# Performance work log

Hardware: AMD Instinct MI355X
Metric: run time of the kernel (lower is better)

The kernel has to match this reference:

```python
import jax, jax.numpy as jnp
import numpy as np

# ---- static config (mirrors init_kwargs) ----
BATCH = 16384
N_SCALARS = 64
N_KERNELS = 32
L2_INDICES = tuple(range(15))
N_L2 = len(L2_INDICES) + 1          # selected kernels + sum-over-kernels
HIDDEN_MIX = 256
HIDDEN_CORR = 128
SILU_NORM = 1.6790                   # e3nn normalize2mom constant for silu

# ---- real-basis Wigner 3j tensors (unit Frobenius norm, as in e3nn) ----
def _su2_gen(l):
    m = np.arange(-l, l + 1)
    d = 2 * l + 1
    Jz = np.diag(m).astype(complex)
    jp = np.sqrt(l * (l + 1) - m[:-1] * (m[:-1] + 1))
    Jp = np.zeros((d, d), complex)
    Jp[np.arange(1, d), np.arange(0, d - 1)] = jp
    Jm = Jp.conj().T
    return (Jp + Jm) / 2, (Jp - Jm) / 2j, Jz

def _real_basis(l):
    d = 2 * l + 1
    U = np.zeros((d, d), complex)
    U[l, l] = 1.0
    for m in range(1, l + 1):
        U[l + m, l + m] = (-1) ** m / np.sqrt(2)
        U[l + m, l - m] = 1 / np.sqrt(2)
        U[l - m, l - m] = 1j / np.sqrt(2)
        U[l - m, l + m] = -1j * (-1) ** m / np.sqrt(2)
    return U

def _real_gens(l):
    if l == 0:
        return [np.zeros((1, 1))] * 3
    U = _real_basis(l)
    return [np.real(U @ (-1j * J) @ U.conj().T) for J in _su2_gen(l)]

def _w3j(l1, l2, l3):
    G1, G2, G3 = _real_gens(l1), _real_gens(l2), _real_gens(l3)
    d1, d2, d3 = 2 * l1 + 1, 2 * l2 + 1, 2 * l3 + 1
    I1, I2, I3 = np.eye(d1), np.eye(d2), np.eye(d3)
    rows = []
    for a in range(3):  # invariance under all 3 so(3) generators
        rows.append(np.kron(np.kron(G1[a], I2), I3)
                    + np.kron(np.kron(I1, G2[a]), I3)
                    + np.kron(np.kron(I1, I2), G3[a]))
    M = np.concatenate(rows, 0)
    _, _, Vh = np.linalg.svd(M)
    c = Vh[-1].reshape(d1, d2, d3)
    c = c / np.linalg.norm(c)
    idx = np.unravel_index(np.argmax(np.abs(c)), c.shape)
    return (c * np.sign(c[idx])).astype(np.float32)

C000 = jnp.asarray(_w3j(0, 0, 0))
C022 = jnp.asarray(_w3j(0, 2, 2))
C202 = jnp.asarray(_w3j(2, 0, 2))
C220 = jnp.asarray(_w3j(2, 2, 0))
C222 = jnp.asarray(_w3j(2, 2, 2))

def _tp_path(w, c, x1, x2):
    # w: [u,v,w], c (wigner 3j): [i,j,k], x1: [b,u,i], x2: [b,v,j] -> [b,w,k]
    return jnp.einsum('uvw,ijk,bui,bvj->bwk', w, c, x1, x2, optimize='optimal')

def _forward(scalars, kernel_t2s, mlp_w1, mlp_w2, mlp_w3, gate_threshold,
             tp1_w000, tp1_w220, tp1_w022, tp1_w202, tp1_w222,
             tp2_w022, tp2_w202, tp2_w222, correction_scale):
    # ---- KernelMixingHead ----
    h = SILU_NORM * jax.nn.silu(scalars @ mlp_w1 / mlp_w1.shape[0] ** 0.5)
    h = SILU_NORM * jax.nn.silu(h @ mlp_w2 / mlp_w2.shape[0] ** 0.5)
    relative = h @ mlp_w3 / mlp_w3.shape[0] ** 0.5          # [B, K]
    magnitude = jnp.linalg.norm(kernel_t2s, axis=-1)         # [B, K]
    gate = magnitude / (magnitude + gate_threshold)
    weights = relative * gate / N_KERNELS ** 0.5
    mixed = jnp.einsum('bk,bkm->bm', weights, kernel_t2s)    # [B, 5]

    # ---- EquivariantCorrectionHead ----
    sel = kernel_t2s[:, jnp.asarray(L2_INDICES), :]          # [B, n_l2-1, 5]
    t = jnp.concatenate([sel, kernel_t2s.sum(axis=1, keepdims=True)], axis=1)  # [B, N_L2, 5]
    xs = scalars[:, :, None]                                 # [B, ns, 1] (0e channels)
    ns, nl, hc = N_SCALARS, N_L2, HIDDEN_CORR
    # e3nn FullyConnectedTensorProduct path norms ('component'/'element')
    a0 = (1.0 / (ns * ns + nl * nl)) ** 0.5
    a2 = (5.0 / (2 * ns * nl + nl * nl)) ** 0.5
    y0 = a0 * (_tp_path(tp1_w000, C000, xs, xs) + _tp_path(tp1_w220, C220, t, t))   # [B,hc,1]
    y2 = a2 * (_tp_path(tp1_w022, C022, xs, t) + _tp_path(tp1_w202, C202, t, xs)
               + _tp_path(tp1_w222, C222, t, t))                                     # [B,hc,5]
    b2 = (5.0 / (3 * hc * hc)) ** 0.5
    corr = b2 * (_tp_path(tp2_w022, C022, y0, y2) + _tp_path(tp2_w202, C202, y2, y0)
                 + _tp_path(tp2_w222, C222, y2, y2))                                 # [B,1,5]
    return mixed + correction_scale * corr[:, 0, :]

def setup_inputs() -> dict:
    key = jax.random.key(0)
    ks = jax.random.split(key, 13)
    f32 = jnp.float32
    return {
        'scalars': jax.random.normal(ks[0], (BATCH, N_SCALARS), f32),
        'kernel_t2s': jax.random.normal(ks[1], (BATCH, N_KERNELS, 5), f32),
        'mlp_w1': jax.random.normal(ks[2], (N_SCALARS, HIDDEN_MIX), f32),
        'mlp_w2': jax.random.normal(ks[3], (HIDDEN_MIX, HIDDEN_MIX), f32),
        'mlp_w3': jax.random.normal(ks[4], (HIDDEN_MIX, N_KERNELS), f32),
        'gate_threshold': jnp.ones((N_KERNELS,), f32),
        'tp1_w000': jax.random.normal(ks[5], (N_SCALARS, N_SCALARS, HIDDEN_CORR), f32),
        'tp1_w220': jax.random.normal(ks[6], (N_L2, N_L2, HIDDEN_CORR), f32),
        'tp1_w022': jax.random.normal(ks[7], (N_SCALARS, N_L2, HIDDEN_CORR), f32),
        'tp1_w202': jax.random.normal(ks[8], (N_L2, N_SCALARS, HIDDEN_CORR), f32),
        'tp1_w222': jax.random.normal(ks[9], (N_L2, N_L2, HIDDEN_CORR), f32),
        'tp2_w022': jax.random.normal(ks[10], (HIDDEN_CORR, HIDDEN_CORR, 1), f32),
        'tp2_w202': jax.random.normal(ks[11], (HIDDEN_CORR, HIDDEN_CORR, 1), f32),
        'tp2_w222': jax.random.normal(ks[12], (HIDDEN_CORR, HIDDEN_CORR, 1), f32),
        'correction_scale': jnp.asarray(0.1, f32),
    }

def reference(scalars, kernel_t2s, mlp_w1, mlp_w2, mlp_w3, gate_threshold,
              tp1_w000, tp1_w220, tp1_w022, tp1_w202, tp1_w222,
              tp2_w022, tp2_w202, tp2_w222, correction_scale):
    return _forward(scalars, kernel_t2s, mlp_w1, mlp_w2, mlp_w3, gate_threshold,
                    tp1_w000, tp1_w220, tp1_w022, tp1_w202, tp1_w222,
                    tp2_w022, tp2_w202, tp2_w222, correction_scale)
```

## Files before the change

kernel.cpp:

```cpp
#include <hip/hip_runtime.h>
#include <hip/hip_bf16.h>
#include <cmath>
#include <complex>
#include <vector>
#include <cstring>
#include <cstdint>


#define C222_FLIP -1.0f

#define MIX_WS_OFF   0
#define W202T_OFF    327680
#define B2H_OFF      393216
#define B2L_OFF      1294336
#define Y0_WS_OFF    2195456
#define Y2P_OFF      10584064

#define NCHUNK2      110

typedef __attribute__((ext_vector_type(8))) short short8;
typedef __attribute__((ext_vector_type(4))) float f32x4;

struct Coefs {
  float c222[125];
  float d022[5];
  float d202[5];
  float d220[5];
  float a0, a2, b2;
};

#define FMA8(acc, wa, wb, sv) do { \
  acc[0] = fmaf((wa).x, (sv), acc[0]); \
  acc[1] = fmaf((wa).y, (sv), acc[1]); \
  acc[2] = fmaf((wa).z, (sv), acc[2]); \
  acc[3] = fmaf((wa).w, (sv), acc[3]); \
  acc[4] = fmaf((wb).x, (sv), acc[4]); \
  acc[5] = fmaf((wb).y, (sv), acc[5]); \
  acc[6] = fmaf((wb).z, (sv), acc[6]); \
  acc[7] = fmaf((wb).w, (sv), acc[7]); \
} while (0)

#define FMA4(acc, wa, sv) do { \
  acc[0] = fmaf((wa).x, (sv), acc[0]); \
  acc[1] = fmaf((wa).y, (sv), acc[1]); \
  acc[2] = fmaf((wa).z, (sv), acc[2]); \
  acc[3] = fmaf((wa).w, (sv), acc[3]); \
} while (0)

__device__ __forceinline__ float act_silu(float x) {
  return 1.679f * x / (1.0f + expf(-x));
}

__device__ __forceinline__ short f2bf(float x) {
  __hip_bfloat16 h = __float2bfloat16(x);
  return *reinterpret_cast<short*>(&h);
}
__device__ __forceinline__ float bf2f(short s) {
  __hip_bfloat16 h = *reinterpret_cast<__hip_bfloat16*>(&s);
  return __bfloat162float(h);
}

__device__ __forceinline__ int bperm(int n, int k) {
  return ((n >> 4) << 9) | (((((k >> 3) << 4) | (n & 15))) << 3) | (k & 7);
}

__global__ __launch_bounds__(256) void k_prep(
    const float* __restrict__ s, const float* __restrict__ t2s,
    const float* __restrict__ w1, const float* __restrict__ w2,
    const float* __restrict__ w3, const float* __restrict__ gthr,
    float* __restrict__ mixed_ws)
{
  __shared__ float sT[64][36];
  __shared__ float hT[256][36];

  const int tid = threadIdx.x;
  const int b0  = blockIdx.x * 32;

  #pragma unroll
  for (int i = 0; i < 8; i++) {
    int flat = tid + i * 256;
    int bl = flat >> 6, k = flat & 63;
    sT[k][bl] = s[(size_t)(b0 + bl) * 64 + k];
  }
  __syncthreads();

  const int cg = tid & 31, bg = tid >> 5;
  const int c0 = cg * 8, bb0 = bg * 4;

  float acc[4][8];
  #pragma unroll
  for (int j = 0; j < 4; j++)
    #pragma unroll
    for (int i = 0; i < 8; i++) acc[j][i] = 0.f;

  for (int k = 0; k < 64; k++) {
    float4 bv = *(const float4*)&sT[k][bb0];
    float4 wa = *(const float4*)&w1[k * 256 + c0];
    float4 wb = *(const float4*)&w1[k * 256 + c0 + 4];
    const float bvv[4] = {bv.x, bv.y, bv.z, bv.w};
    #pragma unroll
    for (int j = 0; j < 4; j++) { FMA8(acc[j], wa, wb, bvv[j]); }
  }
  #pragma unroll
  for (int j = 0; j < 4; j++)
    #pragma unroll
    for (int i = 0; i < 8; i++)
      hT[c0 + i][bb0 + j] = act_silu(acc[j][i] * 0.125f);
  __syncthreads();

  float acc2[4][8];
  #pragma unroll
  for (int j = 0; j < 4; j++)
    #pragma unroll
    for (int i = 0; i < 8; i++) acc2[j][i] = 0.f;

  for (int k = 0; k < 256; k++) {
    float4 bv = *(const float4*)&hT[k][bb0];
    float4 wa = *(const float4*)&w2[k * 256 + c0];
    float4 wb = *(const float4*)&w2[k * 256 + c0 + 4];
    const float bvv[4] = {bv.x, bv.y, bv.z, bv.w};
    #pragma unroll
    for (int j = 0; j < 4; j++) { FMA8(acc2[j], wa, wb, bvv[j]); }
  }
  __syncthreads();
  #pragma unroll
  for (int j = 0; j < 4; j++)
    #pragma unroll
    for (int i = 0; i < 8; i++)
      hT[c0 + i][bb0 + j] = act_silu(acc2[j][i] * 0.0625f);
  __syncthreads();

  const int jj  = tid & 31;
  const int blg = tid >> 5;
  float acc3[4] = {0.f, 0.f, 0.f, 0.f};
  for (int k = 0; k < 256; k++) {
    float wv  = w3[k * 32 + jj];
    float4 hv = *(const float4*)&hT[k][blg * 4];
    acc3[0] = fmaf(hv.x, wv, acc3[0]);
    acc3[1] = fmaf(hv.y, wv, acc3[1]);
    acc3[2] = fmaf(hv.z, wv, acc3[2]);
    acc3[3] = fmaf(hv.w, wv, acc3[3]);
  }
  const float thrv = gthr[jj];
  #pragma unroll
  for (int r = 0; r < 4; r++) {
    int bl = blg * 4 + r;
    int b  = b0 + bl;
    float rel = acc3[r] * 0.0625f;
    const float* tp = t2s + (size_t)(b * 32 + jj) * 5;
    float tv0 = tp[0], tv1 = tp[1], tv2 = tp[2], tv3 = tp[3], tv4 = tp[4];
    float mag  = sqrtf(tv0*tv0 + tv1*tv1 + tv2*tv2 + tv3*tv3 + tv4*tv4);
    float gate = mag / (mag + thrv);
    float w = rel * gate * 0.17677669529663687f;
    float pm0 = w*tv0, pm1 = w*tv1, pm2 = w*tv2, pm3 = w*tv3, pm4 = w*tv4;
    #pragma unroll
    for (int off = 16; off >= 1; off >>= 1) {
      pm0 += __shfl_xor(pm0, off);
      pm1 += __shfl_xor(pm1, off);
      pm2 += __shfl_xor(pm2, off);
      pm3 += __shfl_xor(pm3, off);
      pm4 += __shfl_xor(pm4, off);
    }
    if (jj == 0) {
      float* mp = mixed_ws + (size_t)b * 5;
      mp[0] = pm0; mp[1] = pm1; mp[2] = pm2; mp[3] = pm3; mp[4] = pm4;
    }
  }
}

__global__ __launch_bounds__(256) void k_wprep(
    const float* __restrict__ w000,
    const float* __restrict__ w2202, float* __restrict__ w202T,
    const float* __restrict__ w022, const float* __restrict__ w202,
    const float* __restrict__ w222, const float* __restrict__ w220,
    short* __restrict__ B2h, short* __restrict__ B2l)
{
  const int tid = threadIdx.x;
  const int blk = blockIdx.x;
  if (blk < 64) {
    int u = blk;
    int base = u * 64 - (u * (u - 1)) / 2;
    int n = (64 - u) * 128;
    for (int idx = tid; idx < n; idx += 256) {
      int t = idx >> 7, wc = idx & 127;
      int v = u + t;
      int p = base + t;
      float val = w000[(size_t)(u * 64 + v) * 128 + wc];
      if (v > u) val += w000[(size_t)(v * 64 + u) * 128 + wc];
      size_t off = (size_t)(45 + (p >> 5)) * 4096 + bperm(wc, p & 31);
      short hs = f2bf(val);
      B2h[off] = hs;
      B2l[off] = f2bf(val - bf2f(hs));
    }
  } else if (blk < 128) {
    int idx = (blk - 64) * 256 + tid;
    int u = idx >> 7, v = idx & 127;
    w202T[v * 128 + u] = w2202[u * 128 + v];
  } else {
    int c = blk - 128;
    #pragma unroll
    for (int i = 0; i < 16; i++) {
      int e = i * 256 + tid;
      int nb = e >> 9;
      int ln = (e >> 3) & 63;
      int j  = e & 7;
      int w  = nb * 16 + (ln & 15);
      int kk = ((ln >> 4) << 3) | j;
      float V = 0.f;
      if (c < 32) {
        int v = c >> 1, u = (c & 1) * 32 + kk;
        V = w022[(size_t)(u * 16 + v) * 128 + w]
          + w202[(size_t)(v * 64 + u) * 128 + w];
      } else if (c < 40) {
        int K = (c - 32) * 32 + kk;
        int u = K >> 4, v = K & 15;
        V = w222[(size_t)(u * 16 + v) * 128 + w];
      } else {
        int q = (c - 40) * 32 + kk;
        if (q < 136) {
          int u = 0;
          while ((u + 1) * 16 - ((u + 1) * u) / 2 <= q) u++;
          int base = u * 16 - (u * (u - 1)) / 2;
          int v = u + (q - base);
          V = w220[(size_t)(u * 16 + v) * 128 + w];
          if (v > u) V += w220[(size_t)(v * 16 + u) * 128 + w];
        }
      }
      short hs = f2bf(V);
      B2h[(size_t)c * 4096 + e] = hs;
      B2l[(size_t)c * 4096 + e] = f2bf(V - bf2f(hs));
    }
  }
}

__global__ __launch_bounds__(512) void k_y2a(
    const float* __restrict__ s, const float* __restrict__ t2s,
    const short* __restrict__ B2h, const short* __restrict__ B2l,
    unsigned short* __restrict__ y2p, Coefs cf)
{
  __shared__ float sL[64][68];
  __shared__ float tL[64][81];
  __shared__ __align__(16) short BhL[2][4096];
  __shared__ __align__(16) short BlL[2][4096];
  __shared__ float cL222[125];

  const int tid  = threadIdx.x;
  const int b0   = blockIdx.x * 64;
  const int wave = tid >> 6;
  const int lane = tid & 63;
  const int m16  = lane & 15;
  const int quad = lane >> 4;
  const int bg   = wave & 3;
  const int nh   = wave >> 2;
  const int bloc = bg * 16 + m16;
  const int wbase = nh * 64;

  float dk022[5];
  #pragma unroll
  for (int k = 0; k < 5; k++) dk022[k] = cf.d022[k];

  if (tid == 0) {
    #pragma unroll
    for (int i = 0; i < 125; i++) cL222[i] = cf.c222[i];
  }
  for (int idx = tid; idx < 4096; idx += 512) {
    int bl = idx >> 6, k = idx & 63;
    sL[bl][k] = s[(size_t)(b0 + bl) * 64 + k];
  }
  for (int idx = tid; idx < 5120; idx += 512) {
    int bl = idx / 80, rem = idx - bl * 80;
    int u = rem / 5, m = rem - u * 5;
    int b = b0 + bl;
    float v;
    if (u < 15) v = t2s[(size_t)(b * 32 + u) * 5 + m];
    else {
      v = 0.f;
      for (int kk = 0; kk < 32; kk++) v += t2s[(size_t)(b * 32 + kk) * 5 + m];
    }
    tL[bl][rem] = v;
  }
  __syncthreads();

  ((short8*)BhL[0])[tid] = ((const short8*)B2h)[tid];
  ((short8*)BlL[0])[tid] = ((const short8*)B2l)[tid];
  __syncthreads();

  f32x4 acc[5][4];
  #pragma unroll
  for (int k = 0; k < 5; k++)
    #pragma unroll
    for (int nf = 0; nf < 4; nf++) acc[k][nf] = 0.f;
  f32x4 p[4];
  #pragma unroll
  for (int nf = 0; nf < 4; nf++) p[nf] = 0.f;

  for (int c = 0; c < 40; c++) {
    const int cur = c & 1;
    if (c + 1 < 40) {
      ((short8*)BhL[cur ^ 1])[tid] = ((const short8*)(B2h + (size_t)(c + 1) * 4096))[tid];
      ((short8*)BlL[cur ^ 1])[tid] = ((const short8*)(B2l + (size_t)(c + 1) * 4096))[tid];
    }
    short8 bhv[4], blv[4];
    #pragma unroll
    for (int nf = 0; nf < 4; nf++) {
      const int nb = nh * 4 + nf;
      bhv[nf] = *(const short8*)&BhL[cur][nb * 512 + lane * 8];
      blv[nf] = *(const short8*)&BlL[cur][nb * 512 + lane * 8];
    }

    if (c < 32) {
      const int ks = c & 1;
      float sv[8];
      {
        float4 a = *(const float4*)&sL[bloc][ks * 32 + quad * 8];
        float4 b = *(const float4*)&sL[bloc][ks * 32 + quad * 8 + 4];
        sv[0]=a.x; sv[1]=a.y; sv[2]=a.z; sv[3]=a.w;
        sv[4]=b.x; sv[5]=b.y; sv[6]=b.z; sv[7]=b.w;
      }
      short8 ah, al;
      #pragma unroll
      for (int j = 0; j < 8; j++) {
        float x = sv[j];
        short hs = f2bf(x);
        ah[j] = hs;
        al[j] = f2bf(x - bf2f(hs));
      }
      #pragma unroll
      for (int nf = 0; nf < 4; nf++) {
        p[nf] = __builtin_amdgcn_mfma_f32_16x16x32_bf16(ah, bhv[nf], p[nf], 0, 0, 0);
        p[nf] = __builtin_amdgcn_mfma_f32_16x16x32_bf16(ah, blv[nf], p[nf], 0, 0, 0);
        p[nf] = __builtin_amdgcn_mfma_f32_16x16x32_bf16(al, bhv[nf], p[nf], 0, 0, 0);
      }
      if (ks == 1) {
        const int v = c >> 1;
        #pragma unroll
        for (int r = 0; r < 4; r++) {
          const int bl = bg * 16 + quad * 4 + r;
          const float* tr = &tL[bl][v * 5];
          #pragma unroll
          for (int k = 0; k < 5; k++) {
            float f = dk022[k] * tr[k];
            #pragma unroll
            for (int nf = 0; nf < 4; nf++)
              acc[k][nf][r] += f * p[nf][r];
          }
        }
        #pragma unroll
        for (int nf = 0; nf < 4; nf++) p[nf] = 0.f;
      }
    } else {
      int cc = c - 32;
      int u  = cc * 2 + (quad >> 1);
      int vb = (quad & 1) * 8;
      float tu[5];
      #pragma unroll
      for (int i = 0; i < 5; i++) tu[i] = tL[bloc][u * 5 + i];
      float G[25];
      #pragma unroll
      for (int jk = 0; jk < 25; jk++) {
        float g = 0.f;
        #pragma unroll
        for (int i = 0; i < 5; i++)
          g = fmaf(cL222[i * 25 + jk], tu[i], g);
        G[jk] = g;
      }
      float av[5][8];
      #pragma unroll
      for (int j = 0; j < 8; j++) {
        float t5[5];
        #pragma unroll
        for (int j5 = 0; j5 < 5; j5++) t5[j5] = tL[bloc][(vb + j) * 5 + j5];
        #pragma unroll
        for (int k = 0; k < 5; k++) {
          float q = 0.f;
          #pragma unroll
          for (int j5 = 0; j5 < 5; j5++)
            q = fmaf(G[j5 * 5 + k], t5[j5], q);
          av[k][j] = q;
        }
      }
      #pragma unroll
      for (int k = 0; k < 5; k++) {
        short8 ah, al;
        #pragma unroll
        for (int j = 0; j < 8; j++) {
          float x = av[k][j];
          short hs = f2bf(x);
          ah[j] = hs;
          al[j] = f2bf(x - bf2f(hs));
        }
        #pragma unroll
        for (int nf = 0; nf < 4; nf++) {
          acc[k][nf] = __builtin_amdgcn_mfma_f32_16x16x32_bf16(ah, bhv[nf], acc[k][nf], 0, 0, 0);
          acc[k][nf] = __builtin_amdgcn_mfma_f32_16x16x32_bf16(ah, blv[nf], acc[k][nf], 0, 0, 0);
          acc[k][nf] = __builtin_amdgcn_mfma_f32_16x16x32_bf16(al, bhv[nf], acc[k][nf], 0, 0, 0);
        }
      }
    }
    __syncthreads();
  }

  #pragma unroll
  for (int nf = 0; nf < 4; nf++) {
    int ch = wbase + nf * 16 + m16;
    #pragma unroll
    for (int r = 0; r < 4; r++) {
      int b = b0 + bg * 16 + quad * 4 + r;
      #pragma unroll
      for (int k = 0; k < 5; k++)
        y2p[((size_t)b * 5 + k) * 128 + ch] = (unsigned short)f2bf(acc[k][nf][r]);
    }
  }
}

__global__ __launch_bounds__(512) void k_y0b(
    const float* __restrict__ s, const float* __restrict__ t2s,
    const short* __restrict__ B2h, const short* __restrict__ B2l,
    float* __restrict__ y0w, Coefs cf)
{
  __shared__ float sL[64][68];
  __shared__ float tL[64][81];
  __shared__ __align__(16) short BhL[2][4096];
  __shared__ __align__(16) short BlL[2][4096];
  __shared__ unsigned char p136s[136];
  __shared__ unsigned short p16[2080];

  const int tid  = threadIdx.x;
  const int b0   = blockIdx.x * 64;
  const int wave = tid >> 6;
  const int lane = tid & 63;
  const int m16  = lane & 15;
  const int quad = lane >> 4;
  const int bg   = wave & 3;
  const int nh   = wave >> 2;
  const int bloc = bg * 16 + m16;
  const int wbase = nh * 64;

  float dk220[5];
  #pragma unroll
  for (int k = 0; k < 5; k++) dk220[k] = cf.d220[k];

  for (int idx = tid; idx < 4096; idx += 512) {
    int bl = idx >> 6, k = idx & 63;
    sL[bl][k] = s[(size_t)(b0 + bl) * 64 + k];
  }
  for (int idx = tid; idx < 5120; idx += 512) {
    int bl = idx / 80, rem = idx - bl * 80;
    int u = rem / 5, m = rem - u * 5;
    int b = b0 + bl;
    float v;
    if (u < 15) v = t2s[(size_t)(b * 32 + u) * 5 + m];
    else {
      v = 0.f;
      for (int kk = 0; kk < 32; kk++) v += t2s[(size_t)(b * 32 + kk) * 5 + m];
    }
    tL[bl][rem] = v;
  }
  if (tid < 16) {
    int u = tid;
    int base = u * 16 - (u * (u - 1)) / 2;
    for (int t = 0; t < 16 - u; t++)
      p136s[base + t] = (unsigned char)((u << 4) | (u + t));
  }
  if (tid < 64) {
    int u = tid;
    int base = u * 64 - (u * (u - 1)) / 2;
    for (int t = 0; t < 64 - u; t++)
      p16[base + t] = (unsigned short)((u << 8) | (u + t));
  }
  __syncthreads();

  ((short8*)BhL[0])[tid] = ((const short8*)(B2h + (size_t)40 * 4096))[tid];
  ((short8*)BlL[0])[tid] = ((const short8*)(B2l + (size_t)40 * 4096))[tid];
  __syncthreads();

  f32x4 accY0[4];
  #pragma unroll
  for (int nf = 0; nf < 4; nf++) accY0[nf] = 0.f;

  for (int c = 40; c < NCHUNK2; c++) {
    const int cur = c & 1;
    if (c + 1 < NCHUNK2) {
      ((short8*)BhL[cur ^ 1])[tid] = ((const short8*)(B2h + (size_t)(c + 1) * 4096))[tid];
      ((short8*)BlL[cur ^ 1])[tid] = ((const short8*)(B2l + (size_t)(c + 1) * 4096))[tid];
    }
    short8 bhv[4], blv[4];
    #pragma unroll
    for (int nf = 0; nf < 4; nf++) {
      const int nb = nh * 4 + nf;
      bhv[nf] = *(const short8*)&BhL[cur][nb * 512 + lane * 8];
      blv[nf] = *(const short8*)&BlL[cur][nb * 512 + lane * 8];
    }

    short8 ah, al;
    if (c < 45) {
      int cc = c - 40;
      int qbase = cc * 32 + quad * 8;
      #pragma unroll
      for (int j = 0; j < 8; j++) {
        int q = qbase + j;
        float g = 0.f;
        if (q < 136) {
          int uv = p136s[q];
          int u = uv >> 4, v = uv & 15;
          #pragma unroll
          for (int m = 0; m < 5; m++)
            g = fmaf(dk220[m] * tL[bloc][u * 5 + m], tL[bloc][v * 5 + m], g);
        }
        short hs = f2bf(g);
        ah[j] = hs;
        al[j] = f2bf(g - bf2f(hs));
      }
    } else {
      int pbase = (c - 45) * 32 + quad * 8;
      #pragma unroll
      for (int j = 0; j < 8; j++) {
        int uv = p16[pbase + j];
        float x = sL[bloc][uv >> 8] * sL[bloc][uv & 255];
        short hs = f2bf(x);
        ah[j] = hs;
        al[j] = f2bf(x - bf2f(hs));
      }
    }
    #pragma unroll
    for (int nf = 0; nf < 4; nf++) {
      accY0[nf] = __builtin_amdgcn_mfma_f32_16x16x32_bf16(ah, bhv[nf], accY0[nf], 0, 0, 0);
      accY0[nf] = __builtin_amdgcn_mfma_f32_16x16x32_bf16(ah, blv[nf], accY0[nf], 0, 0, 0);
      accY0[nf] = __builtin_amdgcn_mfma_f32_16x16x32_bf16(al, bhv[nf], accY0[nf], 0, 0, 0);
    }
    __syncthreads();
  }

  #pragma unroll
  for (int nf = 0; nf < 4; nf++) {
    int ch = wbase + nf * 16 + m16;
    #pragma unroll
    for (int r = 0; r < 4; r++) {
      int b = b0 + bg * 16 + quad * 4 + r;
      y0w[(size_t)b * 128 + ch] = accY0[nf][r];
    }
  }
}

__global__ __launch_bounds__(512) void k_fused(
    const float* __restrict__ mixed_ws,
    const float* __restrict__ y0w, const unsigned short* __restrict__ y2p,
    const float* __restrict__ w2022, const float* __restrict__ w202T,
    const float* __restrict__ w2222,
    const float* __restrict__ csc, float* __restrict__ out, Coefs cf)
{
  __shared__ __align__(16) float y0I[16][128][2];
  __shared__ __align__(16) float wLd[32][128];
  __shared__ float y2S[5][16][32][2];
  __shared__ float cL222[125];
  __shared__ float corrAcc[32][5];
  __shared__ float pPL[32][25];

  const int tid = threadIdx.x;
  const int b0  = blockIdx.x * 32;

  float dk022[5], dk202[5];
  #pragma unroll
  for (int k = 0; k < 5; k++) { dk022[k] = cf.d022[k]; dk202[k] = cf.d202[k]; }

  if (tid == 0) {
    #pragma unroll
    for (int i = 0; i < 125; i++) cL222[i] = cf.c222[i];
  }
  for (int idx = tid; idx < 4096; idx += 512) {
    int bl = idx >> 7, ch = idx & 127;
    y0I[bl >> 1][ch][bl & 1] = cf.a0 * y0w[(size_t)(b0 + bl) * 128 + ch];
  }

  const int xw = tid & 31;
  const int g  = tid >> 5;
  const int w0 = xw * 4;
  const int bA = 2 * g, bB = 2 * g + 1;
  const int srow = tid >> 4;
  const int scol = (tid & 15) * 8;

  float y2acc[5][2][4];
  #pragma unroll
  for (int k = 0; k < 5; k++) {
    #pragma unroll
    for (int h = 0; h < 2; h++) {
      int b = b0 + 2 * g + h;
      const unsigned short* yp = y2p + ((size_t)b * 5 + k) * 128 + w0;
      ushort4 u4 = *(const ushort4*)yp;
      y2acc[k][h][0] = cf.a2 * bf2f((short)u4.x);
      y2acc[k][h][1] = cf.a2 * bf2f((short)u4.y);
      y2acc[k][h][2] = cf.a2 * bf2f((short)u4.z);
      y2acc[k][h][3] = cf.a2 * bf2f((short)u4.w);
    }
  }
  __syncthreads();

  {
    float gvr[2][4] = {{0.f,0.f,0.f,0.f},{0.f,0.f,0.f,0.f}};
    for (int t = 0; t < 4; t++) {
      const int u0 = t * 32;
      *(float4*)&wLd[srow][scol]     = *(const float4*)(w2022 + (size_t)(u0 + srow) * 128 + scol);
      *(float4*)&wLd[srow][scol + 4] = *(const float4*)(w2022 + (size_t)(u0 + srow) * 128 + scol + 4);
      __syncthreads();
      #pragma unroll 8
      for (int uu = 0; uu < 32; uu++) {
        float2 y0p = *(const float2*)&y0I[g][u0 + uu][0];
        float4 w4 = *(const float4*)&wLd[uu][w0];
        FMA4(gvr[0], w4, y0p.x);
        FMA4(gvr[1], w4, y0p.y);
      }
      __syncthreads();
    }
    #pragma unroll
    for (int k = 0; k < 5; k++) {
      float pA = gvr[0][0]*y2acc[k][0][0] + gvr[0][1]*y2acc[k][0][1]
               + gvr[0][2]*y2acc[k][0][2] + gvr[0][3]*y2acc[k][0][3];
      float pB = gvr[1][0]*y2acc[k][1][0] + gvr[1][1]*y2acc[k][1][1]
               + gvr[1][2]*y2acc[k][1][2] + gvr[1][3]*y2acc[k][1][3];
      pA += __shfl_xor(pA, 16); pA += __shfl_xor(pA, 8); pA += __shfl_xor(pA, 4);
      pA += __shfl_xor(pA, 2);  pA += __shfl_xor(pA, 1);
      pB += __shfl_xor(pB, 16); pB += __shfl_xor(pB, 8); pB += __shfl_xor(pB, 4);
      pB += __shfl_xor(pB, 2);  pB += __shfl_xor(pB, 1);
      if (xw == 0) {
        corrAcc[bA][k] = dk022[k] * pA;
        corrAcc[bB][k] = dk022[k] * pB;
      }
    }
  }
  {
    float hvr[2][4] = {{0.f,0.f,0.f,0.f},{0.f,0.f,0.f,0.f}};
    for (int t = 0; t < 4; t++) {
      const int u0 = t * 32;
      *(float4*)&wLd[srow][scol]     = *(const float4*)(w202T + (size_t)(u0 + srow) * 128 + scol);
      *(float4*)&wLd[srow][scol + 4] = *(const float4*)(w202T + (size_t)(u0 + srow) * 128 + scol + 4);
      __syncthreads();
      #pragma unroll 8
      for (int uu = 0; uu < 32; uu++) {
        float2 y0p = *(const float2*)&y0I[g][u0 + uu][0];
        float4 w4 = *(const float4*)&wLd[uu][w0];
        FMA4(hvr[0], w4, y0p.x);
        FMA4(hvr[1], w4, y0p.y);
      }
      __syncthreads();
    }
    #pragma unroll
    for (int k = 0; k < 5; k++) {
      float pA = hvr[0][0]*y2acc[k][0][0] + hvr[0][1]*y2acc[k][0][1]
               + hvr[0][2]*y2acc[k][0][2] + hvr[0][3]*y2acc[k][0][3];
      float pB = hvr[1][0]*y2acc[k][1][0] + hvr[1][1]*y2acc[k][1][1]
               + hvr[1][2]*y2acc[k][1][2] + hvr[1][3]*y2acc[k][1][3];
      pA += __shfl_xor(pA, 16); pA += __shfl_xor(pA, 8); pA += __shfl_xor(pA, 4);
      pA += __shfl_xor(pA, 2);  pA += __shfl_xor(pA, 1);
      pB += __shfl_xor(pB, 16); pB += __shfl_xor(pB, 8); pB += __shfl_xor(pB, 4);
      pB += __shfl_xor(pB, 2);  pB += __shfl_xor(pB, 1);
      if (xw == 0) {
        corrAcc[bA][k] += dk202[k] * pA;
        corrAcc[bB][k] += dk202[k] * pB;
      }
    }
  }
  {
    float zr[5][2][4];
    #pragma unroll
    for (int i = 0; i < 5; i++)
      #pragma unroll
      for (int h = 0; h < 2; h++)
        #pragma unroll
        for (int w = 0; w < 4; w++) zr[i][h][w] = 0.f;

    for (int t = 0; t < 4; t++) {
      const int u0 = t * 32;
      *(float4*)&wLd[srow][scol]     = *(const float4*)(w2222 + (size_t)(u0 + srow) * 128 + scol);
      *(float4*)&wLd[srow][scol + 4] = *(const float4*)(w2222 + (size_t)(u0 + srow) * 128 + scol + 4);
      if (w0 >= u0 && w0 < u0 + 32) {
        const int uu0 = w0 - u0;
        #pragma unroll
        for (int i = 0; i < 5; i++)
          #pragma unroll
          for (int h = 0; h < 2; h++)
            #pragma unroll
            for (int c = 0; c < 4; c++)
              y2S[i][g][uu0 + c][h] = y2acc[i][h][c];
      }
      __syncthreads();
      #pragma unroll 4
      for (int uu = 0; uu < 32; uu++) {
        float4 w4 = *(const float4*)&wLd[uu][w0];
        #pragma unroll
        for (int i = 0; i < 5; i++) {
          float ya = y2S[i][g][uu][0];
          float yb = y2S[i][g][uu][1];
          FMA4(zr[i][0], w4, ya);
          FMA4(zr[i][1], w4, yb);
        }
      }
      __syncthreads();
    }
    #pragma unroll
    for (int i = 0; i < 5; i++) {
      #pragma unroll
      for (int j = 0; j < 5; j++) {
        float pA = zr[i][0][0]*y2acc[j][0][0] + zr[i][0][1]*y2acc[j][0][1]
                 + zr[i][0][2]*y2acc[j][0][2] + zr[i][0][3]*y2acc[j][0][3];
        float pB = zr[i][1][0]*y2acc[j][1][0] + zr[i][1][1]*y2acc[j][1][1]
                 + zr[i][1][2]*y2acc[j][1][2] + zr[i][1][3]*y2acc[j][1][3];
        pA += __shfl_xor(pA, 16); pA += __shfl_xor(pA, 8); pA += __shfl_xor(pA, 4);
        pA += __shfl_xor(pA, 2);  pA += __shfl_xor(pA, 1);
        pB += __shfl_xor(pB, 16); pB += __shfl_xor(pB, 8); pB += __shfl_xor(pB, 4);
        pB += __shfl_xor(pB, 2);  pB += __shfl_xor(pB, 1);
        if (xw == 0) {
          pPL[bA][i * 5 + j] = pA;
          pPL[bB][i * 5 + j] = pB;
        }
      }
    }
  }
  __syncthreads();

  if (tid < 160) {
    int bb = tid / 5, k = tid - bb * 5;
    float c2 = 0.f;
    #pragma unroll
    for (int ii = 0; ii < 5; ii++)
      #pragma unroll
      for (int jj = 0; jj < 5; jj++)
        c2 = fmaf(cL222[ii * 25 + jj * 5 + k], pPL[bb][ii * 5 + jj], c2);
    float tot = corrAcc[bb][k] + c2;
    int b = b0 + bb;
    out[(size_t)b * 5 + k] = mixed_ws[(size_t)b * 5 + k] + csc[0] * cf.b2 * tot;
  }
}

namespace {

using cplx = std::complex<double>;

static void su2_gen(int l, std::vector<cplx>& Jx, std::vector<cplx>& Jy,
                    std::vector<cplx>& Jz) {
  int d = 2 * l + 1;
  Jx.assign((size_t)d * d, cplx(0, 0));
  Jy.assign((size_t)d * d, cplx(0, 0));
  Jz.assign((size_t)d * d, cplx(0, 0));
  for (int a = 0; a < d; a++) Jz[(size_t)a * d + a] = cplx(a - l, 0);
  for (int r = 1; r < d; r++) {
    double m = (r - 1) - l;
    double v = std::sqrt(l * (l + 1.0) - m * (m + 1.0));
    Jx[(size_t)r * d + (r - 1)] += cplx(v / 2, 0);
    Jx[(size_t)(r - 1) * d + r] += cplx(v / 2, 0);
    Jy[(size_t)r * d + (r - 1)] += cplx(0, -v / 2);
    Jy[(size_t)(r - 1) * d + r] += cplx(0, v / 2);
  }
}

static void real_basis(int l, std::vector<cplx>& U) {
  int d = 2 * l + 1;
  U.assign((size_t)d * d, cplx(0, 0));
  U[(size_t)l * d + l] = cplx(1, 0);
  double is2 = 1.0 / std::sqrt(2.0);
  for (int m = 1; m <= l; m++) {
    double sgn = (m % 2 == 0) ? 1.0 : -1.0;
    U[(size_t)(l + m) * d + (l + m)] = cplx(sgn * is2, 0);
    U[(size_t)(l + m) * d + (l - m)] = cplx(is2, 0);
    U[(size_t)(l - m) * d + (l - m)] = cplx(0, is2);
    U[(size_t)(l - m) * d + (l + m)] = cplx(0, -sgn * is2);
  }
}

static void real_gens(int l, std::vector<double> G[3]) {
  int d = 2 * l + 1;
  if (l == 0) { for (int a = 0; a < 3; a++) G[a].assign(1, 0.0); return; }
  std::vector<cplx> J[3];
  su2_gen(l, J[0], J[1], J[2]);
  std::vector<cplx> U;
  real_basis(l, U);
  for (int a = 0; a < 3; a++) {
    std::vector<cplx> T((size_t)d * d, cplx(0, 0));
    for (int i = 0; i < d; i++)
      for (int k = 0; k < d; k++) {
        cplx s(0, 0);
        for (int j = 0; j < d; j++)
          s += U[(size_t)i * d + j] * (cplx(0, -1) * J[a][(size_t)j * d + k]);
        T[(size_t)i * d + k] = s;
      }
    G[a].assign((size_t)d * d, 0.0);
    for (int i = 0; i < d; i++)
      for (int k = 0; k < d; k++) {
        cplx s(0, 0);
        for (int j = 0; j < d; j++)
          s += T[(size_t)i * d + j] * std::conj(U[(size_t)k * d + j]);
        G[a][(size_t)i * d + k] = s.real();
      }
  }
}

static void w3j_host(int l1, int l2, int l3, float* out) {
  int d1 = 2 * l1 + 1, d2 = 2 * l2 + 1, d3 = 2 * l3 + 1;
  int D = d1 * d2 * d3;
  std::vector<double> G1[3], G2[3], G3[3];
  real_gens(l1, G1); real_gens(l2, G2); real_gens(l3, G3);
  int R = 3 * D;
  std::vector<double> M((size_t)R * D, 0.0);
  for (int a = 0; a < 3; a++) {
    double* Ma = &M[(size_t)a * D * D];
    for (int i1 = 0; i1 < d1; i1++)
      for (int j1 = 0; j1 < d1; j1++) {
        double g = G1[a][(size_t)i1 * d1 + j1];
        if (g == 0.0) continue;
        for (int i2 = 0; i2 < d2; i2++)
          for (int i3 = 0; i3 < d3; i3++)
            Ma[(size_t)((i1 * d2 + i2) * d3 + i3) * D + ((j1 * d2 + i2) * d3 + i3)] += g;
      }
    for (int i2 = 0; i2 < d2; i2++)
      for (int j2 = 0; j2 < d2; j2++) {
        double g = G2[a][(size_t)i2 * d2 + j2];
        if (g == 0.0) continue;
        for (int i1 = 0; i1 < d1; i1++)
          for (int i3 = 0; i3 < d3; i3++)
            Ma[(size_t)((i1 * d2 + i2) * d3 + i3) * D + ((i1 * d2 + j2) * d3 + i3)] += g;
      }
    for (int i3 = 0; i3 < d3; i3++)
      for (int j3 = 0; j3 < d3; j3++) {
        double g = G3[a][(size_t)i3 * d3 + j3];
        if (g == 0.0) continue;
        for (int i1 = 0; i1 < d1; i1++)
          for (int i2 = 0; i2 < d2; i2++)
            Ma[(size_t)((i1 * d2 + i2) * d3 + i3) * D + ((i1 * d2 + i2) * d3 + j3)] += g;
      }
  }
  std::vector<int> pivcol;
  int rank = 0;
  for (int col = 0; col < D && rank < R; col++) {
    int pr = -1; double pv = 1e-9;
    for (int r = rank; r < R; r++) {
      double av = std::fabs(M[(size_t)r * D + col]);
      if (av > pv) { pv = av; pr = r; }
    }
    if (pr < 0) continue;
    if (pr != rank)
      for (int c = 0; c < D; c++) std::swap(M[(size_t)pr * D + c], M[(size_t)rank * D + c]);
    double inv = 1.0 / M[(size_t)rank * D + col];
    for (int c = 0; c < D; c++) M[(size_t)rank * D + c] *= inv;
    for (int r = 0; r < R; r++) {
      if (r == rank) continue;
      double f = M[(size_t)r * D + col];
      if (f != 0.0)
        for (int c = 0; c < D; c++) M[(size_t)r * D + c] -= f * M[(size_t)rank * D + c];
    }
    pivcol.push_back(col);
    rank++;
  }
  std::vector<char> isp(D, 0);
  for (int c : pivcol) isp[c] = 1;
  int fc = 0;
  for (int c = 0; c < D; c++) if (!isp[c]) { fc = c; break; }
  std::vector<double> x(D, 0.0);
  x[fc] = 1.0;
  for (int r = 0; r < rank; r++) x[pivcol[r]] = -M[(size_t)r * D + fc];
  double n = 0;
  for (double v : x) n += v * v;
  n = std::sqrt(n);
  for (int c = 0; c < D; c++) x[c] /= n;
  double best = 0;
  for (int c = 0; c < D; c++) { double av = std::fabs(x[c]); if (av > best) best = av; }
  double ssum = 0;
  for (int c = 0; c < D; c++) {
    double av = std::fabs(x[c]);
    if (av >= best * 0.999) ssum += (x[c] >= 0 ? 1.0 : -1.0);
  }
  double sgn = (ssum >= 0) ? 1.0 : -1.0;
  for (int c = 0; c < D; c++) out[c] = (float)(x[c] * sgn);
}

}

extern "C" void kernel_launch(void* const* d_in, const int* in_sizes, int n_in,
                              void* d_out, int out_size, void* d_ws, size_t ws_size,
                              hipStream_t stream)
{
  (void)in_sizes; (void)n_in; (void)out_size; (void)ws_size;

  const float* s     = (const float*)d_in[0];
  const float* t2s   = (const float*)d_in[1];
  const float* w1    = (const float*)d_in[2];
  const float* w2    = (const float*)d_in[3];
  const float* w3    = (const float*)d_in[4];
  const float* gthr  = (const float*)d_in[5];
  const float* w000  = (const float*)d_in[6];
  const float* w220  = (const float*)d_in[7];
  const float* w022  = (const float*)d_in[8];
  const float* w202  = (const float*)d_in[9];
  const float* w222  = (const float*)d_in[10];
  const float* w2022 = (const float*)d_in[11];
  const float* w2202 = (const float*)d_in[12];
  const float* w2222 = (const float*)d_in[13];
  const float* csc   = (const float*)d_in[14];
  float* out = (float*)d_out;

  char* ws = (char*)d_ws;
  float* mixed_ws = (float*)(ws + MIX_WS_OFF);
  float* w202T    = (float*)(ws + W202T_OFF);
  short* B2h      = (short*)(ws + B2H_OFF);
  short* B2l      = (short*)(ws + B2L_OFF);
  float* y0_ws    = (float*)(ws + Y0_WS_OFF);
  unsigned short* y2p = (unsigned short*)(ws + Y2P_OFF);

  Coefs cf;
  {
    float c000v[1], c022v[25], c202v[25], c220v[25];
    w3j_host(0, 0, 0, c000v);
    w3j_host(0, 2, 2, c022v);
    w3j_host(2, 0, 2, c202v);
    w3j_host(2, 2, 0, c220v);
    w3j_host(2, 2, 2, cf.c222);
    for (int i = 0; i < 125; i++) cf.c222[i] *= C222_FLIP;
    for (int k = 0; k < 5; k++) {
      cf.d022[k] = c022v[k * 5 + k];
      cf.d202[k] = c202v[k * 5 + k];
      cf.d220[k] = c220v[k * 5 + k];
    }
    (void)c000v;
    cf.a0 = (float)std::sqrt(1.0 / (64.0 * 64.0 + 16.0 * 16.0));
    cf.a2 = (float)std::sqrt(5.0 / (2.0 * 64.0 * 16.0 + 16.0 * 16.0));
    cf.b2 = (float)std::sqrt(5.0 / (3.0 * 128.0 * 128.0));
  }

  hipLaunchKernelGGL(k_prep, dim3(512), dim3(256), 0, stream,
                     s, t2s, w1, w2, w3, gthr, mixed_ws);
  hipLaunchKernelGGL(k_wprep, dim3(173), dim3(256), 0, stream,
                     w000, w2202, w202T,
                     w022, w202, w222, w220, B2h, B2l);
  hipLaunchKernelGGL(k_y0b, dim3(256), dim3(512), 0, stream,
                     s, t2s, B2h, B2l, y0_ws, cf);
  hipLaunchKernelGGL(k_y2a, dim3(256), dim3(512), 0, stream,
                     s, t2s, B2h, B2l, y2p, cf);
  hipLaunchKernelGGL(k_fused, dim3(512), dim3(512), 0, stream,
                     mixed_ws, y0_ws, y2p, w2022, w202T, w2222, csc, out, cf);
}
```

Baseline: 403.4 us.

## Halve k_y0b batch tile, double grid, load B fragments directly from global

The y0 GEMM kernel now handles 32 batch rows per block instead of 64, so the grid doubles to 512 blocks. Each wave covers 32 output channels with two accumulators instead of four. The double-buffered LDS staging of B2h/B2l and the per-chunk __syncthreads are removed, and each wave reads its B fragments straight from global memory (L2-resident). The aim is more parallelism across CUs and no block-wide barriers, at the cost of more redundant global B reads and A-fragment recomputation per output.

```diff
diff --git a/kernel.cpp b/kernel.cpp
--- a/kernel.cpp
+++ b/kernel.cpp
@@ -418,33 +418,31 @@
     const short* __restrict__ B2h, const short* __restrict__ B2l,
     float* __restrict__ y0w, Coefs cf)
 {
-  __shared__ float sL[64][68];
-  __shared__ float tL[64][81];
-  __shared__ __align__(16) short BhL[2][4096];
-  __shared__ __align__(16) short BlL[2][4096];
+  __shared__ float sL[32][65];
+  __shared__ float tL[32][81];
   __shared__ unsigned char p136s[136];
   __shared__ unsigned short p16[2080];
 
   const int tid  = threadIdx.x;
-  const int b0   = blockIdx.x * 64;
+  const int b0   = blockIdx.x * 32;
   const int wave = tid >> 6;
   const int lane = tid & 63;
   const int m16  = lane & 15;
   const int quad = lane >> 4;
-  const int bg   = wave & 3;
-  const int nh   = wave >> 2;
+  const int bg   = wave & 1;
+  const int nh   = wave >> 1;
   const int bloc = bg * 16 + m16;
-  const int wbase = nh * 64;
+  const int wbase = nh * 32;
 
   float dk220[5];
   #pragma unroll
   for (int k = 0; k < 5; k++) dk220[k] = cf.d220[k];
 
-  for (int idx = tid; idx < 4096; idx += 512) {
+  for (int idx = tid; idx < 2048; idx += 512) {
     int bl = idx >> 6, k = idx & 63;
     sL[bl][k] = s[(size_t)(b0 + bl) * 64 + k];
   }
-  for (int idx = tid; idx < 5120; idx += 512) {
+  for (int idx = tid; idx < 2560; idx += 512) {
     int bl = idx / 80, rem = idx - bl * 80;
     int u = rem / 5, m = rem - u * 5;
     int b = b0 + bl;
@@ -470,27 +468,20 @@
   }
   __syncthreads();
 
-  ((short8*)BhL[0])[tid] = ((const short8*)(B2h + (size_t)40 * 4096))[tid];
-  ((short8*)BlL[0])[tid] = ((const short8*)(B2l + (size_t)40 * 4096))[tid];
-  __syncthreads();
-
-  f32x4 accY0[4];
-  #pragma unroll
-  for (int nf = 0; nf < 4; nf++) accY0[nf] = 0.f;
+  f32x4 accY0[2];
+  accY0[0] = 0.f; accY0[1] = 0.f;
+
+  const short8* Bh8 = (const short8*)B2h;
+  const short8* Bl8 = (const short8*)B2l;
+  const int off0 = (nh * 2) * 64 + lane;
+  const int off1 = off0 + 64;
 
   for (int c = 40; c < NCHUNK2; c++) {
-    const int cur = c & 1;
-    if (c + 1 < NCHUNK2) {
-      ((short8*)BhL[cur ^ 1])[tid] = ((const short8*)(B2h + (size_t)(c + 1) * 4096))[tid];
-      ((short8*)BlL[cur ^ 1])[tid] = ((const short8*)(B2l + (size_t)(c + 1) * 4096))[tid];
-    }
-    short8 bhv[4], blv[4];
-    #pragma unroll
-    for (int nf = 0; nf < 4; nf++) {
-      const int nb = nh * 4 + nf;
-      bhv[nf] = *(const short8*)&BhL[cur][nb * 512 + lane * 8];
-      blv[nf] = *(const short8*)&BlL[cur][nb * 512 + lane * 8];
-    }
+    const size_t cb = (size_t)c * 512;
+    short8 bh0 = Bh8[cb + off0];
+    short8 bh1 = Bh8[cb + off1];
+    short8 bl0 = Bl8[cb + off0];
+    short8 bl1 = Bl8[cb + off1];
 
     short8 ah, al;
     if (c < 45) {
@@ -522,17 +513,16 @@
         al[j] = f2bf(x - bf2f(hs));
       }
     }
-    #pragma unroll
-    for (int nf = 0; nf < 4; nf++) {
-      accY0[nf] = __builtin_amdgcn_mfma_f32_16x16x32_bf16(ah, bhv[nf], accY0[nf], 0, 0, 0);
-      accY0[nf] = __builtin_amdgcn_mfma_f32_16x16x32_bf16(ah, blv[nf], accY0[nf], 0, 0, 0);
-      accY0[nf] = __builtin_amdgcn_mfma_f32_16x16x32_bf16(al, bhv[nf], accY0[nf], 0, 0, 0);
-    }
-    __syncthreads();
-  }
-
-  #pragma unroll
-  for (int nf = 0; nf < 4; nf++) {
+    accY0[0] = __builtin_amdgcn_mfma_f32_16x16x32_bf16(ah, bh0, accY0[0], 0, 0, 0);
+    accY0[0] = __builtin_amdgcn_mfma_f32_16x16x32_bf16(ah, bl0, accY0[0], 0, 0, 0);
+    accY0[0] = __builtin_amdgcn_mfma_f32_16x16x32_bf16(al, bh0, accY0[0], 0, 0, 0);
+    accY0[1] = __builtin_amdgcn_mfma_f32_16x16x32_bf16(ah, bh1, accY0[1], 0, 0, 0);
+    accY0[1] = __builtin_amdgcn_mfma_f32_16x16x32_bf16(ah, bl1, accY0[1], 0, 0, 0);
+    accY0[1] = __builtin_amdgcn_mfma_f32_16x16x32_bf16(al, bh1, accY0[1], 0, 0, 0);
+  }
+
+  #pragma unroll
+  for (int nf = 0; nf < 2; nf++) {
     int ch = wbase + nf * 16 + m16;
     #pragma unroll
     for (int r = 0; r < 4; r++) {
@@ -929,7 +919,7 @@
   hipLaunchKernelGGL(k_wprep, dim3(173), dim3(256), 0, stream,
                      w000, w2202, w202T,
                      w022, w202, w222, w220, B2h, B2l);
-  hipLaunchKernelGGL(k_y0b, dim3(256), dim3(512), 0, stream,
+  hipLaunchKernelGGL(k_y0b, dim3(512), dim3(512), 0, stream,
                      s, t2s, B2h, B2l, y0_ws, cf);
   hipLaunchKernelGGL(k_y2a, dim3(256), dim3(512), 0, stream,
                      s, t2s, B2h, B2l, y2p, cf);
```

New measurement: 388.9 us. 1.04x faster.
